# Kernel optimization log

Measured on AMD Instinct MI355X. Metric: run time of the kernel, lower is better.

Reference implementation:

```python
import jax, jax.numpy as jnp
import numpy as np

N = 50000

def gcn_conv(x, src, dst, W, b, num_nodes):
    # x: [N, Fin], src/dst: [E'] (self-loops already included)
    h = x @ W  # [N, Fout]
    ones = jnp.ones(src.shape[0], dtype=h.dtype)
    deg = jax.ops.segment_sum(ones, dst, num_segments=num_nodes)  # in-degree incl. self-loop
    dinv = jnp.where(deg > 0, jax.lax.rsqrt(deg), 0.0)
    norm = dinv[src] * dinv[dst]  # [E']
    msg = h[src] * norm[:, None]  # gather + scale
    out = jax.ops.segment_sum(msg, dst, num_segments=num_nodes)  # scatter-add
    return out + b

def setup_inputs() -> dict:
    key = jax.random.key(0)
    k1, k2, k3, k4, k5, k6 = jax.random.split(key, 6)
    E = 800000
    Fin, H, Fout = 128, 64, 32
    x = jax.random.normal(k1, (N, Fin), dtype=jnp.float32)
    edge_index = jax.random.randint(k2, (2, E), 0, N, dtype=jnp.int32)
    edge_attr = jax.random.normal(k3, (E, 8), dtype=jnp.float32)
    s1 = 1.0 / np.sqrt(Fin)
    s2 = 1.0 / np.sqrt(H)
    W1 = jax.random.uniform(k4, (Fin, H), dtype=jnp.float32, minval=-s1, maxval=s1)
    b1 = jnp.zeros((H,), dtype=jnp.float32)
    W2 = jax.random.uniform(k5, (H, Fout), dtype=jnp.float32, minval=-s2, maxval=s2)
    b2 = jnp.zeros((Fout,), dtype=jnp.float32)
    return {"x": x, "edge_index": edge_index, "edge_attr": edge_attr,
            "W1": W1, "b1": b1, "W2": W2, "b2": b2}

def reference(x, edge_index, edge_attr, W1, b1, W2, b2):
    num_nodes = x.shape[0]
    loop = jnp.arange(num_nodes, dtype=edge_index.dtype)
    src = jnp.concatenate([edge_index[0], loop])
    dst = jnp.concatenate([edge_index[1], loop])
    h = gcn_conv(x, src, dst, W1, b1, num_nodes)
    h = jax.nn.relu(h)
    # dropout is identity in eval mode
    out = gcn_conv(h, src, dst, W2, b2, num_nodes)
    return out
```

## Files before the change

### kernel.cpp

```cpp
#include <hip/hip_runtime.h>
#include <hip/hip_fp16.h>
#include <cstdint>
#include <cstddef>


#define SHIFT 8
#define NPB 256
#define CHUNK 4096
#define CAP 8192
#define CAPSHIFT 13
#define IMG_CAP 6144

__global__ __launch_bounds__(256) void scatter_local_kernel(
    const int* __restrict__ src, const int* __restrict__ dst, int E, int B,
    int* __restrict__ gcur, unsigned* __restrict__ keys) {
  __shared__ int loffs[256], cur[256], gb[256];
  __shared__ int wsum[4];
  __shared__ unsigned image[CHUNK];
  int t = threadIdx.x, w = blockIdx.x;
  int lane = t & 63, wid = t >> 6;
  cur[t] = 0;
  __syncthreads();
  int beg = w * CHUNK, end = min(beg + CHUNK, E);
  for (int i = beg + t; i < end; i += 256) atomicAdd(&cur[dst[i] >> SHIFT], 1);
  __syncthreads();
  {
    int v = cur[t];
    int x = v;
#pragma unroll
    for (int o = 1; o < 64; o <<= 1) { int y = __shfl_up(x, o, 64); if (lane >= o) x += y; }
    if (lane == 63) wsum[wid] = x;
    __syncthreads();
    int bw = 0;
    for (int i = 0; i < wid; ++i) bw += wsum[i];
    int excl = bw + x - v;
    loffs[t] = excl;
    cur[t] = excl;
  }
  __syncthreads();
  for (int i = beg + t; i < end; i += 256) {
    int d = dst[i], s = src[i];
    int b = d >> SHIFT;
    int p = atomicAdd(&cur[b], 1);
    image[p] = ((unsigned)b << 24) | ((unsigned)(d & (NPB - 1)) << 16) | (unsigned)s;
  }
  __syncthreads();
  if (t < B) {
    int c = cur[t] - loffs[t];
    gb[t] = (c > 0) ? atomicAdd(&gcur[t], c) : 0;
  }
  __syncthreads();
  int n = end - beg;
  for (int i = t; i < n; i += 256) {
    unsigned k = image[i];
    int b = (int)(k >> 24);
    int pos = gb[b] + (i - loffs[b]);
    if (pos < CAP) keys[((size_t)b << CAPSHIFT) + pos] = k;
  }
}

__global__ __launch_bounds__(256) void bucket_build_kernel(const unsigned* __restrict__ keys,
                                                           const int* __restrict__ gcur, int N,
                                                           unsigned short* __restrict__ csr,
                                                           int* __restrict__ eoff,
                                                           int* __restrict__ ecnt,
                                                           float* __restrict__ dinv) {
  __shared__ int cnt[NPB], loffs[NPB], cur[NPB];
  __shared__ int image[IMG_CAP];
  int b = blockIdx.x, t = threadIdx.x;
  int m = min(gcur[b], CAP);
  size_t kbase = (size_t)b << CAPSHIFT;
  int nb = b << SHIFT;
  int nn = min(NPB, N - nb);
  cnt[t] = 0;
  __syncthreads();
  for (int i = t; i < m; i += 256) atomicAdd(&cnt[(keys[kbase + i] >> 16) & 0xFF], 1);
  __syncthreads();
  if (t < 64) {
    int v0 = cnt[4 * t], v1 = cnt[4 * t + 1], v2 = cnt[4 * t + 2], v3 = cnt[4 * t + 3];
    int s = v0 + v1 + v2 + v3, x = s;
#pragma unroll
    for (int o = 1; o < 64; o <<= 1) { int y = __shfl_up(x, o, 64); if (t >= o) x += y; }
    int e = x - s;
    loffs[4 * t] = e;                 cur[4 * t] = e;
    loffs[4 * t + 1] = e + v0;        cur[4 * t + 1] = e + v0;
    loffs[4 * t + 2] = e + v0 + v1;   cur[4 * t + 2] = e + v0 + v1;
    loffs[4 * t + 3] = e + v0 + v1 + v2; cur[4 * t + 3] = e + v0 + v1 + v2;
  }
  __syncthreads();
  for (int n2 = t; n2 < nn; n2 += 256) {
    eoff[nb + n2] = (int)kbase + loffs[n2];
    ecnt[nb + n2] = cnt[n2];
    dinv[nb + n2] = 1.0f / sqrtf((float)(cnt[n2] + 1));
  }
  if (m <= IMG_CAP) {
    for (int i = t; i < m; i += 256) {
      unsigned k = keys[kbase + i];
      int p = atomicAdd(&cur[(k >> 16) & 0xFF], 1);
      image[p] = (int)(k & 0xFFFFu);
    }
    __syncthreads();
    for (int i = t; i < m; i += 256) csr[kbase + i] = (unsigned short)image[i];
  } else {
    for (int i = t; i < m; i += 256) {
      unsigned k = keys[kbase + i];
      int p = atomicAdd(&cur[(k >> 16) & 0xFF], 1);
      csr[kbase + p] = (unsigned short)(k & 0xFFFFu);
    }
  }
}

__global__ __launch_bounds__(256) void gemm1_kernel(
    const float* __restrict__ x, const float* __restrict__ W1,
    const float* __restrict__ dinv, __half* __restrict__ h1s, int N) {
  __shared__ float ws[128 * 64];
  __shared__ float xs[64 * 128];
  const int t = threadIdx.x;
  const int rowBase = blockIdx.x * 64;
  float4* ws4 = (float4*)ws;
  float4* xs4 = (float4*)xs;
  for (int i = t; i < 128 * 16; i += 256) ws4[i] = ((const float4*)W1)[i];
  for (int i = t; i < 64 * 32; i += 256) {
    int r = i >> 5, kq = i & 31;
    int row = rowBase + r;
    float4 v = make_float4(0.f, 0.f, 0.f, 0.f);
    if (row < N) v = ((const float4*)x)[(size_t)row * 32 + kq];
    xs4[r * 32 + (kq ^ ((r >> 2) & 7))] = v;
  }
  __syncthreads();
  const int g = t & 15;
  const int rg = t >> 4;
  const int swz = rg & 7;
  float acc[4][4] = {};
  for (int kq = 0; kq < 32; ++kq) {
    float4 a[4];
#pragma unroll
    for (int j = 0; j < 4; ++j) a[j] = xs4[(4 * rg + j) * 32 + (kq ^ swz)];
    float4 w[4];
#pragma unroll
    for (int kk = 0; kk < 4; ++kk) w[kk] = ws4[(4 * kq + kk) * 16 + g];
#pragma unroll
    for (int j = 0; j < 4; ++j) {
      acc[j][0] += a[j].x * w[0].x + a[j].y * w[1].x + a[j].z * w[2].x + a[j].w * w[3].x;
      acc[j][1] += a[j].x * w[0].y + a[j].y * w[1].y + a[j].z * w[2].y + a[j].w * w[3].y;
      acc[j][2] += a[j].x * w[0].z + a[j].y * w[1].z + a[j].z * w[2].z + a[j].w * w[3].z;
      acc[j][3] += a[j].x * w[0].w + a[j].y * w[1].w + a[j].z * w[2].w + a[j].w * w[3].w;
    }
  }
#pragma unroll
  for (int j = 0; j < 4; ++j) {
    int row = rowBase + 4 * rg + j;
    if (row < N) {
      float dv = dinv[row];
      union { __half2 h2[2]; float2 f2v; } u;
      u.h2[0] = __floats2half2_rn(acc[j][0] * dv, acc[j][1] * dv);
      u.h2[1] = __floats2half2_rn(acc[j][2] * dv, acc[j][3] * dv);
      ((float2*)h1s)[(size_t)row * 16 + g] = u.f2v;
    }
  }
}

__device__ __forceinline__ float4 unpack4(float2 raw) {
  union { float2 f2v; __half2 h2[2]; } u; u.f2v = raw;
  float2 lo = __half22float2(u.h2[0]), hi = __half22float2(u.h2[1]);
  return make_float4(lo.x, lo.y, hi.x, hi.y);
}
__device__ __forceinline__ void acc4(float4& a, const float4& v) {
  a.x += v.x; a.y += v.y; a.z += v.z; a.w += v.w;
}

__global__ __launch_bounds__(256) void gather64_gemm2_kernel(
    const __half* __restrict__ h1s, const unsigned short* __restrict__ csr,
    const int* __restrict__ eoff, const int* __restrict__ ecnt,
    const float* __restrict__ dinv, const float* __restrict__ b1,
    const float* __restrict__ W2, __half* __restrict__ h2s, int N) {
  __shared__ float w2s[64 * 32];
  __shared__ float arow[16 * 68];
  int t = threadIdx.x;
  float4* w2s4 = (float4*)w2s;
  for (int i = t; i < 512; i += 256) w2s4[i] = ((const float4*)W2)[i];
  __syncthreads();
  int slot = t >> 4;
  int d = blockIdx.x * 16 + slot;
  if (d >= N) return;
  int f = t & 15;
  const float2* h1p = (const float2*)h1s;
  int beg = eoff[d], m = ecnt[d];
  float4 a0 = unpack4(h1p[(size_t)d * 16 + f]);
  float4 aA = make_float4(0.f, 0.f, 0.f, 0.f);
  float4 aB = make_float4(0.f, 0.f, 0.f, 0.f);
  float4 aC = make_float4(0.f, 0.f, 0.f, 0.f);
  int j = 0;
  for (; j + 16 <= m; j += 16) {
    int s_[16];
#pragma unroll
    for (int i = 0; i < 16; ++i) s_[i] = csr[beg + j + i];
    float2 v_[16];
#pragma unroll
    for (int i = 0; i < 16; ++i) v_[i] = h1p[(size_t)s_[i] * 16 + f];
#pragma unroll
    for (int i = 0; i < 16; ++i) {
      float4 v = unpack4(v_[i]);
      float4* ac = (i & 3) == 0 ? &a0 : (i & 3) == 1 ? &aA : (i & 3) == 2 ? &aB : &aC;
      acc4(*ac, v);
    }
  }
  if (j < m) {
    int s_[16];
#pragma unroll
    for (int i = 0; i < 16; ++i) { int jj = j + i; s_[i] = csr[beg + (jj < m ? jj : m - 1)]; }
    float2 v_[16];
#pragma unroll
    for (int i = 0; i < 16; ++i) v_[i] = h1p[(size_t)s_[i] * 16 + f];
#pragma unroll
    for (int i = 0; i < 16; ++i) {
      float4 v = unpack4(v_[i]);
      bool ok = (j + i < m);
      float4 vm = make_float4(ok ? v.x : 0.f, ok ? v.y : 0.f, ok ? v.z : 0.f, ok ? v.w : 0.f);
      float4* ac = (i & 3) == 0 ? &a0 : (i & 3) == 1 ? &aA : (i & 3) == 2 ? &aB : &aC;
      acc4(*ac, vm);
    }
  }
  float g0 = (a0.x + aA.x) + (aB.x + aC.x);
  float g1 = (a0.y + aA.y) + (aB.y + aC.y);
  float g2 = (a0.z + aA.z) + (aB.z + aC.z);
  float g3 = (a0.w + aA.w) + (aB.w + aC.w);
  float dv = dinv[d];
  float4 bb = ((const float4*)b1)[f];
  float4 a1v;
  a1v.x = fmaxf(g0 * dv + bb.x, 0.f);
  a1v.y = fmaxf(g1 * dv + bb.y, 0.f);
  a1v.z = fmaxf(g2 * dv + bb.z, 0.f);
  a1v.w = fmaxf(g3 * dv + bb.w, 0.f);
  ((float4*)arow)[slot * 17 + f] = a1v;
  const float* ar = &arow[slot * 68];
  float s0 = 0.f, s1 = 0.f;
#pragma unroll
  for (int kk = 0; kk < 64; ++kk) {
    float a = ar[kk];
    float2 wv = ((const float2*)w2s)[kk * 16 + f];
    s0 += a * wv.x; s1 += a * wv.y;
  }
  ((__half2*)h2s)[(size_t)d * 16 + f] = __floats2half2_rn(s0 * dv, s1 * dv);
}

__global__ __launch_bounds__(256) void gather32_kernel(
    const __half* __restrict__ h2s, const unsigned short* __restrict__ csr,
    const int* __restrict__ eoff, const int* __restrict__ ecnt,
    const float* __restrict__ dinv, const float* __restrict__ b2,
    float* __restrict__ out, int N) {
  int t = threadIdx.x;
  int d = blockIdx.x * 32 + (t >> 3);
  if (d >= N) return;
  int f = t & 7;
  const float2* h2p = (const float2*)h2s;
  int beg = eoff[d], m = ecnt[d];
  float4 a0 = unpack4(h2p[(size_t)d * 8 + f]);
  float4 aA = make_float4(0.f, 0.f, 0.f, 0.f);
  float4 aB = make_float4(0.f, 0.f, 0.f, 0.f);
  float4 aC = make_float4(0.f, 0.f, 0.f, 0.f);
  int j = 0;
  for (; j + 16 <= m; j += 16) {
    int s_[16];
#pragma unroll
    for (int i = 0; i < 16; ++i) s_[i] = csr[beg + j + i];
    float2 v_[16];
#pragma unroll
    for (int i = 0; i < 16; ++i) v_[i] = h2p[(size_t)s_[i] * 8 + f];
#pragma unroll
    for (int i = 0; i < 16; ++i) {
      float4 v = unpack4(v_[i]);
      float4* ac = (i & 3) == 0 ? &a0 : (i & 3) == 1 ? &aA : (i & 3) == 2 ? &aB : &aC;
      acc4(*ac, v);
    }
  }
  if (j < m) {
    int s_[16];
#pragma unroll
    for (int i = 0; i < 16; ++i) { int jj = j + i; s_[i] = csr[beg + (jj < m ? jj : m - 1)]; }
    float2 v_[16];
#pragma unroll
    for (int i = 0; i < 16; ++i) v_[i] = h2p[(size_t)s_[i] * 8 + f];
#pragma unroll
    for (int i = 0; i < 16; ++i) {
      float4 v = unpack4(v_[i]);
      bool ok = (j + i < m);
      float4 vm = make_float4(ok ? v.x : 0.f, ok ? v.y : 0.f, ok ? v.z : 0.f, ok ? v.w : 0.f);
      float4* ac = (i & 3) == 0 ? &a0 : (i & 3) == 1 ? &aA : (i & 3) == 2 ? &aB : &aC;
      acc4(*ac, vm);
    }
  }
  float g0 = (a0.x + aA.x) + (aB.x + aC.x);
  float g1 = (a0.y + aA.y) + (aB.y + aC.y);
  float g2 = (a0.z + aA.z) + (aB.z + aC.z);
  float g3 = (a0.w + aA.w) + (aB.w + aC.w);
  float dv = dinv[d];
  float4 bb = ((const float4*)b2)[f];
  float4 o = make_float4(g0 * dv + bb.x, g1 * dv + bb.y, g2 * dv + bb.z, g3 * dv + bb.w);
  ((float4*)out)[(size_t)d * 8 + f] = o;
}

extern "C" void kernel_launch(void* const* d_in, const int* in_sizes, int n_in,
                              void* d_out, int out_size, void* d_ws, size_t ws_size,
                              hipStream_t stream) {
  const float* x = (const float*)d_in[0];
  const int* edge_index = (const int*)d_in[1];
  const float* W1 = (const float*)d_in[3];
  const float* b1 = (const float*)d_in[4];
  const float* W2 = (const float*)d_in[5];
  const float* b2 = (const float*)d_in[6];
  float* out = (float*)d_out;

  const int N = in_sizes[0] / 128;
  const int E = in_sizes[1] / 2;
  const int* src = edge_index;
  const int* dst = edge_index + E;

  const int B = (N + NPB - 1) >> SHIFT;
  const int nWG = (E + CHUNK - 1) / CHUNK;

  char* ws = (char*)d_ws;
  size_t off = 0;
  auto alloc = [&](size_t bytes) -> void* {
    void* p = ws + off;
    off += (bytes + 255) & ~(size_t)255;
    return p;
  };
  unsigned* keys = (unsigned*)alloc((size_t)B * CAP * 4);
  unsigned short* csr = (unsigned short*)alloc((size_t)B * CAP * 2);
  int* gcur = (int*)alloc((size_t)B * 4);
  int* eoff = (int*)alloc((size_t)N * 4);
  int* ecnt = (int*)alloc((size_t)N * 4);
  float* dinv = (float*)alloc((size_t)N * 4);
  __half* h1s = (__half*)alloc((size_t)N * 64 * 2);
  __half* h2s = (__half*)alloc((size_t)N * 32 * 2);

  hipMemsetAsync(gcur, 0, (size_t)B * 4, stream);
  scatter_local_kernel<<<nWG, 256, 0, stream>>>(src, dst, E, B, gcur, keys);
  bucket_build_kernel<<<B, 256, 0, stream>>>(keys, gcur, N, csr, eoff, ecnt, dinv);
  gemm1_kernel<<<(N + 63) / 64, 256, 0, stream>>>(x, W1, dinv, h1s, N);
  gather64_gemm2_kernel<<<(N + 15) / 16, 256, 0, stream>>>(h1s, csr, eoff, ecnt, dinv, b1, W2, h2s, N);
  gather32_kernel<<<(N + 31) / 32, 256, 0, stream>>>(h2s, csr, eoff, ecnt, dinv, b2, out, N);
}
```

Before: 90.34 us.

## Fuse sort/build and both gather stages into cooperative kernels with grid sync

Merges the scatter and bucket-build kernels into one cooperative launch separated by grid.sync(), and does the same for the two gather kernels, which now use grid-stride persistent loops. The goal is to remove kernel launch gaps and inter-kernel drain/fill overhead between dependent stages. In exchange it adds per-call host queries of device properties and occupancy, a grid-wide barrier, and reduced parallelism in the persistent gather loops. Non-cooperative fallbacks are kept.

```diff
diff --git a/kernel.cpp b/kernel.cpp
--- a/kernel.cpp
+++ b/kernel.cpp
@@ -1,7 +1,10 @@
 #include <hip/hip_runtime.h>
+#include <hip/hip_cooperative_groups.h>
 #include <hip/hip_fp16.h>
 #include <cstdint>
 #include <cstddef>
+
+namespace cg = cooperative_groups;
 
 
 #define SHIFT 8
@@ -11,14 +14,17 @@
 #define CAPSHIFT 13
 #define IMG_CAP 6144
 
-__global__ __launch_bounds__(256) void scatter_local_kernel(
-    const int* __restrict__ src, const int* __restrict__ dst, int E, int B,
-    int* __restrict__ gcur, unsigned* __restrict__ keys) {
+
+__device__ __forceinline__ void sort_phase(const int* __restrict__ src,
+                                           const int* __restrict__ dst, int E, int B,
+                                           int* __restrict__ gcur, unsigned* __restrict__ keys) {
   __shared__ int loffs[256], cur[256], gb[256];
   __shared__ int wsum[4];
   __shared__ unsigned image[CHUNK];
   int t = threadIdx.x, w = blockIdx.x;
   int lane = t & 63, wid = t >> 6;
+  int nWG = (E + CHUNK - 1) / CHUNK;
+  if (w >= nWG) return;
   cur[t] = 0;
   __syncthreads();
   int beg = w * CHUNK, end = min(beg + CHUNK, E);
@@ -59,15 +65,15 @@
   }
 }
 
-__global__ __launch_bounds__(256) void bucket_build_kernel(const unsigned* __restrict__ keys,
-                                                           const int* __restrict__ gcur, int N,
-                                                           unsigned short* __restrict__ csr,
-                                                           int* __restrict__ eoff,
-                                                           int* __restrict__ ecnt,
-                                                           float* __restrict__ dinv) {
+__device__ __forceinline__ void build_phase(const unsigned* __restrict__ keys,
+                                            const int* __restrict__ gcur, int B, int N,
+                                            unsigned short* __restrict__ csr,
+                                            int* __restrict__ eoff, int* __restrict__ ecnt,
+                                            float* __restrict__ dinv) {
   __shared__ int cnt[NPB], loffs[NPB], cur[NPB];
   __shared__ int image[IMG_CAP];
   int b = blockIdx.x, t = threadIdx.x;
+  if (b >= B) return;
   int m = min(gcur[b], CAP);
   size_t kbase = (size_t)b << CAPSHIFT;
   int nb = b << SHIFT;
@@ -108,6 +114,206 @@
       csr[kbase + p] = (unsigned short)(k & 0xFFFFu);
     }
   }
+}
+
+__device__ __forceinline__ float4 unpack4(float2 raw) {
+  union { float2 f2v; __half2 h2[2]; } u; u.f2v = raw;
+  float2 lo = __half22float2(u.h2[0]), hi = __half22float2(u.h2[1]);
+  return make_float4(lo.x, lo.y, hi.x, hi.y);
+}
+__device__ __forceinline__ void acc4(float4& a, const float4& v) {
+  a.x += v.x; a.y += v.y; a.z += v.z; a.w += v.w;
+}
+
+__device__ __forceinline__ void gather1_phase(
+    const __half* __restrict__ h1s, const unsigned short* __restrict__ csr,
+    const int* __restrict__ eoff, const int* __restrict__ ecnt,
+    const float* __restrict__ dinv, const float* __restrict__ b1,
+    const float* __restrict__ W2, __half* __restrict__ h2s, int N) {
+  __shared__ float w2s[64 * 32];
+  __shared__ float arow[16 * 68];
+  int t = threadIdx.x;
+  int G = gridDim.x;
+  float4* w2s4 = (float4*)w2s;
+  for (int i = t; i < 512; i += 256) w2s4[i] = ((const float4*)W2)[i];
+  __syncthreads();
+  int slot = t >> 4;
+  int f = t & 15;
+  const float2* h1p = (const float2*)h1s;
+  for (int d0 = blockIdx.x * 16; d0 < N; d0 += G * 16) {
+    int d = d0 + slot;
+    if (d < N) {
+      int beg = eoff[d], m = ecnt[d];
+      float4 a0 = unpack4(h1p[(size_t)d * 16 + f]);
+      float4 aA = make_float4(0.f, 0.f, 0.f, 0.f);
+      float4 aB = make_float4(0.f, 0.f, 0.f, 0.f);
+      float4 aC = make_float4(0.f, 0.f, 0.f, 0.f);
+      int j = 0;
+      for (; j + 16 <= m; j += 16) {
+        int s_[16];
+#pragma unroll
+        for (int i = 0; i < 16; ++i) s_[i] = csr[beg + j + i];
+        float2 v_[16];
+#pragma unroll
+        for (int i = 0; i < 16; ++i) v_[i] = h1p[(size_t)s_[i] * 16 + f];
+#pragma unroll
+        for (int i = 0; i < 16; ++i) {
+          float4 v = unpack4(v_[i]);
+          float4* ac = (i & 3) == 0 ? &a0 : (i & 3) == 1 ? &aA : (i & 3) == 2 ? &aB : &aC;
+          acc4(*ac, v);
+        }
+      }
+      if (j < m) {
+        int s_[16];
+#pragma unroll
+        for (int i = 0; i < 16; ++i) { int jj = j + i; s_[i] = csr[beg + (jj < m ? jj : m - 1)]; }
+        float2 v_[16];
+#pragma unroll
+        for (int i = 0; i < 16; ++i) v_[i] = h1p[(size_t)s_[i] * 16 + f];
+#pragma unroll
+        for (int i = 0; i < 16; ++i) {
+          float4 v = unpack4(v_[i]);
+          bool ok = (j + i < m);
+          float4 vm = make_float4(ok ? v.x : 0.f, ok ? v.y : 0.f, ok ? v.z : 0.f, ok ? v.w : 0.f);
+          float4* ac = (i & 3) == 0 ? &a0 : (i & 3) == 1 ? &aA : (i & 3) == 2 ? &aB : &aC;
+          acc4(*ac, vm);
+        }
+      }
+      float g0 = (a0.x + aA.x) + (aB.x + aC.x);
+      float g1 = (a0.y + aA.y) + (aB.y + aC.y);
+      float g2 = (a0.z + aA.z) + (aB.z + aC.z);
+      float g3 = (a0.w + aA.w) + (aB.w + aC.w);
+      float dv = dinv[d];
+      float4 bb = ((const float4*)b1)[f];
+      float4 a1v;
+      a1v.x = fmaxf(g0 * dv + bb.x, 0.f);
+      a1v.y = fmaxf(g1 * dv + bb.y, 0.f);
+      a1v.z = fmaxf(g2 * dv + bb.z, 0.f);
+      a1v.w = fmaxf(g3 * dv + bb.w, 0.f);
+      ((float4*)arow)[slot * 17 + f] = a1v;
+      const float* ar = &arow[slot * 68];
+      float s0 = 0.f, s1 = 0.f;
+#pragma unroll
+      for (int kk = 0; kk < 64; ++kk) {
+        float a = ar[kk];
+        float2 wv = ((const float2*)w2s)[kk * 16 + f];
+        s0 += a * wv.x; s1 += a * wv.y;
+      }
+      ((__half2*)h2s)[(size_t)d * 16 + f] = __floats2half2_rn(s0 * dv, s1 * dv);
+    }
+  }
+}
+
+__device__ __forceinline__ void gather2_phase(
+    const __half* __restrict__ h2s, const unsigned short* __restrict__ csr,
+    const int* __restrict__ eoff, const int* __restrict__ ecnt,
+    const float* __restrict__ dinv, const float* __restrict__ b2,
+    float* __restrict__ out, int N) {
+  int t = threadIdx.x;
+  int G = gridDim.x;
+  int f = t & 7;
+  const float2* h2p = (const float2*)h2s;
+  for (int d0 = blockIdx.x * 32; d0 < N; d0 += G * 32) {
+    int d = d0 + (t >> 3);
+    if (d < N) {
+      int beg = eoff[d], m = ecnt[d];
+      float4 a0 = unpack4(h2p[(size_t)d * 8 + f]);
+      float4 aA = make_float4(0.f, 0.f, 0.f, 0.f);
+      float4 aB = make_float4(0.f, 0.f, 0.f, 0.f);
+      float4 aC = make_float4(0.f, 0.f, 0.f, 0.f);
+      int j = 0;
+      for (; j + 16 <= m; j += 16) {
+        int s_[16];
+#pragma unroll
+        for (int i = 0; i < 16; ++i) s_[i] = csr[beg + j + i];
+        float2 v_[16];
+#pragma unroll
+        for (int i = 0; i < 16; ++i) v_[i] = h2p[(size_t)s_[i] * 8 + f];
+#pragma unroll
+        for (int i = 0; i < 16; ++i) {
+          float4 v = unpack4(v_[i]);
+          float4* ac = (i & 3) == 0 ? &a0 : (i & 3) == 1 ? &aA : (i & 3) == 2 ? &aB : &aC;
+          acc4(*ac, v);
+        }
+      }
+      if (j < m) {
+        int s_[16];
+#pragma unroll
+        for (int i = 0; i < 16; ++i) { int jj = j + i; s_[i] = csr[beg + (jj < m ? jj : m - 1)]; }
+        float2 v_[16];
+#pragma unroll
+        for (int i = 0; i < 16; ++i) v_[i] = h2p[(size_t)s_[i] * 8 + f];
+#pragma unroll
+        for (int i = 0; i < 16; ++i) {
+          float4 v = unpack4(v_[i]);
+          bool ok = (j + i < m);
+          float4 vm = make_float4(ok ? v.x : 0.f, ok ? v.y : 0.f, ok ? v.z : 0.f, ok ? v.w : 0.f);
+          float4* ac = (i & 3) == 0 ? &a0 : (i & 3) == 1 ? &aA : (i & 3) == 2 ? &aB : &aC;
+          acc4(*ac, vm);
+        }
+      }
+      float g0 = (a0.x + aA.x) + (aB.x + aC.x);
+      float g1 = (a0.y + aA.y) + (aB.y + aC.y);
+      float g2 = (a0.z + aA.z) + (aB.z + aC.z);
+      float g3 = (a0.w + aA.w) + (aB.w + aC.w);
+      float dv = dinv[d];
+      float4 bb = ((const float4*)b2)[f];
+      float4 o = make_float4(g0 * dv + bb.x, g1 * dv + bb.y, g2 * dv + bb.z, g3 * dv + bb.w);
+      ((float4*)out)[(size_t)d * 8 + f] = o;
+    }
+  }
+}
+
+
+__global__ __launch_bounds__(256) void coop_sort_k(
+    const int* __restrict__ src, const int* __restrict__ dst, int E, int B, int N,
+    int* __restrict__ gcur, unsigned* __restrict__ keys, unsigned short* __restrict__ csr,
+    int* __restrict__ eoff, int* __restrict__ ecnt, float* __restrict__ dinv) {
+  cg::grid_group grid = cg::this_grid();
+  sort_phase(src, dst, E, B, gcur, keys);
+  grid.sync();
+  build_phase(keys, gcur, B, N, csr, eoff, ecnt, dinv);
+}
+
+__global__ __launch_bounds__(256) void scatter_k(
+    const int* __restrict__ src, const int* __restrict__ dst, int E, int B,
+    int* __restrict__ gcur, unsigned* __restrict__ keys) {
+  sort_phase(src, dst, E, B, gcur, keys);
+}
+
+__global__ __launch_bounds__(256) void build_k(
+    const unsigned* __restrict__ keys, const int* __restrict__ gcur, int B, int N,
+    unsigned short* __restrict__ csr, int* __restrict__ eoff, int* __restrict__ ecnt,
+    float* __restrict__ dinv) {
+  build_phase(keys, gcur, B, N, csr, eoff, ecnt, dinv);
+}
+
+__global__ __launch_bounds__(256) void coop_gather_k(
+    const __half* __restrict__ h1s, const unsigned short* __restrict__ csr,
+    const int* __restrict__ eoff, const int* __restrict__ ecnt,
+    const float* __restrict__ dinv, const float* __restrict__ b1,
+    const float* __restrict__ W2, __half* __restrict__ h2s,
+    const float* __restrict__ b2, float* __restrict__ out, int N) {
+  cg::grid_group grid = cg::this_grid();
+  gather1_phase(h1s, csr, eoff, ecnt, dinv, b1, W2, h2s, N);
+  grid.sync();
+  gather2_phase(h2s, csr, eoff, ecnt, dinv, b2, out, N);
+}
+
+__global__ __launch_bounds__(256) void gath1_k(
+    const __half* __restrict__ h1s, const unsigned short* __restrict__ csr,
+    const int* __restrict__ eoff, const int* __restrict__ ecnt,
+    const float* __restrict__ dinv, const float* __restrict__ b1,
+    const float* __restrict__ W2, __half* __restrict__ h2s, int N) {
+  gather1_phase(h1s, csr, eoff, ecnt, dinv, b1, W2, h2s, N);
+}
+
+__global__ __launch_bounds__(256) void gath2_k(
+    const __half* __restrict__ h2s, const unsigned short* __restrict__ csr,
+    const int* __restrict__ eoff, const int* __restrict__ ecnt,
+    const float* __restrict__ dinv, const float* __restrict__ b2,
+    float* __restrict__ out, int N) {
+  gather2_phase(h2s, csr, eoff, ecnt, dinv, b2, out, N);
 }
 
 __global__ __launch_bounds__(256) void gemm1_kernel(
@@ -160,146 +366,6 @@
   }
 }
 
-__device__ __forceinline__ float4 unpack4(float2 raw) {
-  union { float2 f2v; __half2 h2[2]; } u; u.f2v = raw;
-  float2 lo = __half22float2(u.h2[0]), hi = __half22float2(u.h2[1]);
-  return make_float4(lo.x, lo.y, hi.x, hi.y);
-}
-__device__ __forceinline__ void acc4(float4& a, const float4& v) {
-  a.x += v.x; a.y += v.y; a.z += v.z; a.w += v.w;
-}
-
-__global__ __launch_bounds__(256) void gather64_gemm2_kernel(
-    const __half* __restrict__ h1s, const unsigned short* __restrict__ csr,
-    const int* __restrict__ eoff, const int* __restrict__ ecnt,
-    const float* __restrict__ dinv, const float* __restrict__ b1,
-    const float* __restrict__ W2, __half* __restrict__ h2s, int N) {
-  __shared__ float w2s[64 * 32];
-  __shared__ float arow[16 * 68];
-  int t = threadIdx.x;
-  float4* w2s4 = (float4*)w2s;
-  for (int i = t; i < 512; i += 256) w2s4[i] = ((const float4*)W2)[i];
-  __syncthreads();
-  int slot = t >> 4;
-  int d = blockIdx.x * 16 + slot;
-  if (d >= N) return;
-  int f = t & 15;
-  const float2* h1p = (const float2*)h1s;
-  int beg = eoff[d], m = ecnt[d];
-  float4 a0 = unpack4(h1p[(size_t)d * 16 + f]);
-  float4 aA = make_float4(0.f, 0.f, 0.f, 0.f);
-  float4 aB = make_float4(0.f, 0.f, 0.f, 0.f);
-  float4 aC = make_float4(0.f, 0.f, 0.f, 0.f);
-  int j = 0;
-  for (; j + 16 <= m; j += 16) {
-    int s_[16];
-#pragma unroll
-    for (int i = 0; i < 16; ++i) s_[i] = csr[beg + j + i];
-    float2 v_[16];
-#pragma unroll
-    for (int i = 0; i < 16; ++i) v_[i] = h1p[(size_t)s_[i] * 16 + f];
-#pragma unroll
-    for (int i = 0; i < 16; ++i) {
-      float4 v = unpack4(v_[i]);
-      float4* ac = (i & 3) == 0 ? &a0 : (i & 3) == 1 ? &aA : (i & 3) == 2 ? &aB : &aC;
-      acc4(*ac, v);
-    }
-  }
-  if (j < m) {
-    int s_[16];
-#pragma unroll
-    for (int i = 0; i < 16; ++i) { int jj = j + i; s_[i] = csr[beg + (jj < m ? jj : m - 1)]; }
-    float2 v_[16];
-#pragma unroll
-    for (int i = 0; i < 16; ++i) v_[i] = h1p[(size_t)s_[i] * 16 + f];
-#pragma unroll
-    for (int i = 0; i < 16; ++i) {
-      float4 v = unpack4(v_[i]);
-      bool ok = (j + i < m);
-      float4 vm = make_float4(ok ? v.x : 0.f, ok ? v.y : 0.f, ok ? v.z : 0.f, ok ? v.w : 0.f);
-      float4* ac = (i & 3) == 0 ? &a0 : (i & 3) == 1 ? &aA : (i & 3) == 2 ? &aB : &aC;
-      acc4(*ac, vm);
-    }
-  }
-  float g0 = (a0.x + aA.x) + (aB.x + aC.x);
-  float g1 = (a0.y + aA.y) + (aB.y + aC.y);
-  float g2 = (a0.z + aA.z) + (aB.z + aC.z);
-  float g3 = (a0.w + aA.w) + (aB.w + aC.w);
-  float dv = dinv[d];
-  float4 bb = ((const float4*)b1)[f];
-  float4 a1v;
-  a1v.x = fmaxf(g0 * dv + bb.x, 0.f);
-  a1v.y = fmaxf(g1 * dv + bb.y, 0.f);
-  a1v.z = fmaxf(g2 * dv + bb.z, 0.f);
-  a1v.w = fmaxf(g3 * dv + bb.w, 0.f);
-  ((float4*)arow)[slot * 17 + f] = a1v;
-  const float* ar = &arow[slot * 68];
-  float s0 = 0.f, s1 = 0.f;
-#pragma unroll
-  for (int kk = 0; kk < 64; ++kk) {
-    float a = ar[kk];
-    float2 wv = ((const float2*)w2s)[kk * 16 + f];
-    s0 += a * wv.x; s1 += a * wv.y;
-  }
-  ((__half2*)h2s)[(size_t)d * 16 + f] = __floats2half2_rn(s0 * dv, s1 * dv);
-}
-
-__global__ __launch_bounds__(256) void gather32_kernel(
-    const __half* __restrict__ h2s, const unsigned short* __restrict__ csr,
-    const int* __restrict__ eoff, const int* __restrict__ ecnt,
-    const float* __restrict__ dinv, const float* __restrict__ b2,
-    float* __restrict__ out, int N) {
-  int t = threadIdx.x;
-  int d = blockIdx.x * 32 + (t >> 3);
-  if (d >= N) return;
-  int f = t & 7;
-  const float2* h2p = (const float2*)h2s;
-  int beg = eoff[d], m = ecnt[d];
-  float4 a0 = unpack4(h2p[(size_t)d * 8 + f]);
-  float4 aA = make_float4(0.f, 0.f, 0.f, 0.f);
-  float4 aB = make_float4(0.f, 0.f, 0.f, 0.f);
-  float4 aC = make_float4(0.f, 0.f, 0.f, 0.f);
-  int j = 0;
-  for (; j + 16 <= m; j += 16) {
-    int s_[16];
-#pragma unroll
-    for (int i = 0; i < 16; ++i) s_[i] = csr[beg + j + i];
-    float2 v_[16];
-#pragma unroll
-    for (int i = 0; i < 16; ++i) v_[i] = h2p[(size_t)s_[i] * 8 + f];
-#pragma unroll
-    for (int i = 0; i < 16; ++i) {
-      float4 v = unpack4(v_[i]);
-      float4* ac = (i & 3) == 0 ? &a0 : (i & 3) == 1 ? &aA : (i & 3) == 2 ? &aB : &aC;
-      acc4(*ac, v);
-    }
-  }
-  if (j < m) {
-    int s_[16];
-#pragma unroll
-    for (int i = 0; i < 16; ++i) { int jj = j + i; s_[i] = csr[beg + (jj < m ? jj : m - 1)]; }
-    float2 v_[16];
-#pragma unroll
-    for (int i = 0; i < 16; ++i) v_[i] = h2p[(size_t)s_[i] * 8 + f];
-#pragma unroll
-    for (int i = 0; i < 16; ++i) {
-      float4 v = unpack4(v_[i]);
-      bool ok = (j + i < m);
-      float4 vm = make_float4(ok ? v.x : 0.f, ok ? v.y : 0.f, ok ? v.z : 0.f, ok ? v.w : 0.f);
-      float4* ac = (i & 3) == 0 ? &a0 : (i & 3) == 1 ? &aA : (i & 3) == 2 ? &aB : &aC;
-      acc4(*ac, vm);
-    }
-  }
-  float g0 = (a0.x + aA.x) + (aB.x + aC.x);
-  float g1 = (a0.y + aA.y) + (aB.y + aC.y);
-  float g2 = (a0.z + aA.z) + (aB.z + aC.z);
-  float g3 = (a0.w + aA.w) + (aB.w + aC.w);
-  float dv = dinv[d];
-  float4 bb = ((const float4*)b2)[f];
-  float4 o = make_float4(g0 * dv + bb.x, g1 * dv + bb.y, g2 * dv + bb.z, g3 * dv + bb.w);
-  ((float4*)out)[(size_t)d * 8 + f] = o;
-}
-
 extern "C" void kernel_launch(void* const* d_in, const int* in_sizes, int n_in,
                               void* d_out, int out_size, void* d_ws, size_t ws_size,
                               hipStream_t stream) {
@@ -311,12 +377,12 @@
   const float* b2 = (const float*)d_in[6];
   float* out = (float*)d_out;
 
-  const int N = in_sizes[0] / 128;
-  const int E = in_sizes[1] / 2;
+  int N = in_sizes[0] / 128;
+  int E = in_sizes[1] / 2;
   const int* src = edge_index;
   const int* dst = edge_index + E;
 
-  const int B = (N + NPB - 1) >> SHIFT;
+  int B = (N + NPB - 1) >> SHIFT;
   const int nWG = (E + CHUNK - 1) / CHUNK;
 
   char* ws = (char*)d_ws;
@@ -336,9 +402,44 @@
   __half* h2s = (__half*)alloc((size_t)N * 32 * 2);
 
   hipMemsetAsync(gcur, 0, (size_t)B * 4, stream);
-  scatter_local_kernel<<<nWG, 256, 0, stream>>>(src, dst, E, B, gcur, keys);
-  bucket_build_kernel<<<B, 256, 0, stream>>>(keys, gcur, N, csr, eoff, ecnt, dinv);
+
+  int numCU = 256;
+  {
+    int dev = 0;
+    hipDeviceProp_t prop;
+    if (hipGetDevice(&dev) == hipSuccess && hipGetDeviceProperties(&prop, dev) == hipSuccess)
+      numCU = prop.multiProcessorCount;
+  }
+
+  int grid1 = (nWG > B) ? nWG : B;
+  int mb1 = 0;
+  bool coop1_ok = (hipOccupancyMaxActiveBlocksPerMultiprocessor(&mb1, coop_sort_k, 256, 0) == hipSuccess)
+                  && (mb1 * numCU >= grid1);
+  hipError_t e1 = hipErrorUnknown;
+  if (coop1_ok) {
+    void* args1[] = {&src, &dst, &E, &B, &N, &gcur, &keys, &csr, &eoff, &ecnt, &dinv};
+    e1 = hipLaunchCooperativeKernel((void*)coop_sort_k, dim3(grid1), dim3(256), args1, 0, stream);
+  }
+  if (e1 != hipSuccess) {
+    scatter_k<<<nWG, 256, 0, stream>>>(src, dst, E, B, gcur, keys);
+    build_k<<<B, 256, 0, stream>>>(keys, gcur, B, N, csr, eoff, ecnt, dinv);
+  }
+
   gemm1_kernel<<<(N + 63) / 64, 256, 0, stream>>>(x, W1, dinv, h1s, N);
-  gather64_gemm2_kernel<<<(N + 15) / 16, 256, 0, stream>>>(h1s, csr, eoff, ecnt, dinv, b1, W2, h2s, N);
-  gather32_kernel<<<(N + 31) / 32, 256, 0, stream>>>(h2s, csr, eoff, ecnt, dinv, b2, out, N);
-}
+
+  int mb2 = 0;
+  bool q2_ok = (hipOccupancyMaxActiveBlocksPerMultiprocessor(&mb2, coop_gather_k, 256, 0) == hipSuccess)
+               && (mb2 >= 1);
+  hipError_t e2 = hipErrorUnknown;
+  if (q2_ok) {
+    int grid2 = mb2 * numCU;
+    int need = (N + 15) / 16;
+    if (grid2 > need) grid2 = need;
+    void* args2[] = {&h1s, &csr, &eoff, &ecnt, &dinv, &b1, &W2, &h2s, &b2, &out, &N};
+    e2 = hipLaunchCooperativeKernel((void*)coop_gather_k, dim3(grid2), dim3(256), args2, 0, stream);
+  }
+  if (e2 != hipSuccess) {
+    gath1_k<<<(N + 15) / 16, 256, 0, stream>>>(h1s, csr, eoff, ecnt, dinv, b1, W2, h2s, N);
+    gath2_k<<<(N + 31) / 32, 256, 0, stream>>>(h2s, csr, eoff, ecnt, dinv, b2, out, N);
+  }
+}
```

Measured after the change: 196.9 us. 2.18x slower.
